# Performance work log

Hardware: AMD Instinct MI355X
Metric: run time of the kernel (lower is better)

Reference implementation:

```python
import jax, jax.numpy as jnp
import numpy as np

GRID_SIZE = 16          # number of spline intervals; G+1 = 17 control points
KH, KW = 3, 3           # kernel size
EPS = 1e-8


def _extract_patches(x, kh, kw):
    """x: (B,H,W,C) -> patches (B,Ho,Wo,C,kh,kw), valid padding, stride 1."""
    B, H, W, C = x.shape
    Ho, Wo = H - kh + 1, W - kw + 1
    rows = []
    for i in range(kh):
        cols = []
        for j in range(kw):
            cols.append(x[:, i:i + Ho, j:j + Wo, :])  # (B,Ho,Wo,C)
        rows.append(jnp.stack(cols, axis=-1))          # (B,Ho,Wo,C,kw)
    return jnp.stack(rows, axis=-2)                    # (B,Ho,Wo,C,kh,kw)


def setup_inputs() -> dict:
    key = jax.random.key(0)
    k1, k2, k3, k4 = jax.random.split(key, 4)
    B, H, W, C, F = 4, 66, 66, 32, 64
    x = jax.random.normal(k1, (B, H, W, C), dtype=jnp.float32)
    control_points = jax.random.normal(k2, (F, C, KH, KW, GRID_SIZE + 1), dtype=jnp.float32) * 0.1
    w_spline = jax.random.normal(k3, (F, C, KH, KW), dtype=jnp.float32) * 0.1
    w_silu = jax.random.normal(k4, (F, C, KH, KW), dtype=jnp.float32) * 0.1
    bias = jnp.zeros((F,), dtype=jnp.float32)
    return {"x": x, "control_points": control_points, "w_spline": w_spline,
            "w_silu": w_silu, "bias": bias}


def reference(x, control_points, w_spline, w_silu, bias):
    # Fixed B-spline grid in [-1, 1]
    grid = jnp.linspace(-1.0, 1.0, GRID_SIZE + 1, dtype=x.dtype)  # (G+1,)
    grid_spacing = 2.0 / GRID_SIZE

    # Patch extraction (valid padding, stride 1)
    patches = _extract_patches(x, KH, KW)  # (B,Ho,Wo,C,kh,kw)

    # Linear B-spline (hat) basis with normalization
    xc = jnp.clip(patches, -1.0, 1.0)
    dist = jnp.abs(xc[..., None] - grid)                     # (B,Ho,Wo,C,kh,kw,G+1)
    w = jnp.maximum(0.0, 1.0 - dist / grid_spacing)
    basis = w / (jnp.sum(w, axis=-1, keepdims=True) + EPS)

    # K(x) = w_spline * spline(x) + w_silu * SiLU(x); reduce over (C,kh,kw) per filter
    cp_eff = w_spline[..., None] * control_points            # (F,C,kh,kw,G+1)
    spline_term = jnp.einsum('bhwcijg,fcijg->bhwf', basis, cp_eff)
    silu_term = jnp.einsum('bhwcij,fcij->bhwf', jax.nn.silu(patches), w_silu)

    return spline_term + silu_term + bias  # (B,Ho,Wo,F)
```

## Files before the change

### kernel.cpp

```cpp
#include <hip/hip_runtime.h>
#include <stdint.h>

typedef _Float16 half8 __attribute__((ext_vector_type(8)));
typedef float f32x16 __attribute__((ext_vector_type(16)));

#define NPX  (4 * 66 * 66 * 32)
#define NTH  (3 * 64 * 1728)
#define TH_OFF_BYTES ((size_t)NPX * 18 * 2)
#define PREP_BLOCKS  ((NPX + NTH) / 256)

__global__ __launch_bounds__(256) void kan_prep(
    const float* __restrict__ x, const float* __restrict__ cp,
    const float* __restrict__ wspl, const float* __restrict__ wsil,
    _Float16* __restrict__ Ff, _Float16* __restrict__ th)
{
    int tid = blockIdx.x * 256 + threadIdx.x;
    if (tid < NPX) {
        float p  = x[tid];
        float xc = fminf(1.0f, fmaxf(-1.0f, p));
        float u  = fmaf(xc, 8.0f, 8.0f);
        union { _Float16 h[18]; uint32_t w[9]; } pk;
#pragma unroll
        for (int m = 0; m < 17; ++m)
            pk.h[m] = (_Float16)fmaxf(0.0f, 1.0f - fabsf(u - (float)m));
        pk.h[17] = (_Float16)(p * __builtin_amdgcn_rcpf(1.0f + __expf(-p)));
        uint32_t* dst = (uint32_t*)(Ff + (size_t)tid * 18);
#pragma unroll
        for (int q = 0; q < 9; ++q) dst[q] = pk.w[q];
    } else if (tid < NPX + NTH) {
        int e  = tid - NPX;
        int k  = e % 1728;
        int fi = e / 1728;
        int f  = fi & 63;
        int i  = fi >> 6;
        int j  = k / 576;
        int q  = k - j * 576;
        int c  = q / 18;
        int m  = q - c * 18;
        int base = ((f * 32 + c) * 3 + i) * 3 + j;
        float v = (m < 17) ? wspl[base] * cp[base * 17 + m] : wsil[base];
        th[e] = (_Float16)v;
    }
}

__global__ __launch_bounds__(128) void kan_main(
    const _Float16* __restrict__ Ff, const _Float16* __restrict__ th,
    const float* __restrict__ bias, float* __restrict__ out)
{
    __shared__ _Float16 lA[2][64 * 72];
    __shared__ _Float16 lB[2][64 * 72];

    const int bx = blockIdx.x;
    const int i  = blockIdx.y;
    const int b  = bx >> 6;
    const int ho = bx & 63;
    const int tid  = threadIdx.x;
    const int wv   = tid >> 6;
    const int lane = tid & 63;
    const int spx   = tid >> 1;
    const int shalf = tid & 1;

    const size_t Abase = (size_t)((b * 66 + ho + i) * 66) * 576;
    const size_t Bbase = (size_t)(i * 64 + spx) * 1728;

    uint4 pfA0, pfA1, pfA2, pfA3, pfB0, pfB1, pfB2, pfB3;
#define LOADCH(ch)                                                             \
    {                                                                          \
        int j_  = (ch) / 9;                                                    \
        int qo_ = ((ch) - j_ * 9) * 64;                                        \
        const uint4* ga = (const uint4*)(Ff + Abase + (size_t)(spx + j_) * 576 \
                                         + qo_ + shalf * 32);                  \
        pfA0 = ga[0]; pfA1 = ga[1]; pfA2 = ga[2]; pfA3 = ga[3];                \
        const uint4* gb = (const uint4*)(th + Bbase + (ch) * 64 + shalf * 32); \
        pfB0 = gb[0]; pfB1 = gb[1]; pfB2 = gb[2]; pfB3 = gb[3];                \
    }

    LOADCH(0)

    const int r31 = lane & 31, kh = lane >> 5;
    f32x16 acc0, acc1;
    {
        float b0v = (i == 1) ? bias[r31] : 0.0f;
        float b1v = (i == 1) ? bias[32 + r31] : 0.0f;
#pragma unroll
        for (int r = 0; r < 16; ++r) { acc0[r] = b0v; acc1[r] = b1v; }
    }

    const int aoff  = (wv * 32 + r31) * 72 + kh * 8;
    const int boff0 = r31 * 72 + kh * 8;
    const int boff1 = (32 + r31) * 72 + kh * 8;
    char* wbA = (char*)lA[0] + spx * 144 + shalf * 64;
    char* wbB = (char*)lB[0] + spx * 144 + shalf * 64;

    int cur = 0;
    for (int ch = 0; ch < 27; ++ch) {
        uint4* wA = (uint4*)(wbA + cur * 9216);
        uint4* wB = (uint4*)(wbB + cur * 9216);
        wA[0] = pfA0; wA[1] = pfA1; wA[2] = pfA2; wA[3] = pfA3;
        wB[0] = pfB0; wB[1] = pfB1; wB[2] = pfB2; wB[3] = pfB3;
        __syncthreads();
        if (ch < 26) LOADCH(ch + 1)
        const _Float16* pa  = lA[cur] + aoff;
        const _Float16* pb0 = lB[cur] + boff0;
        const _Float16* pb1 = lB[cur] + boff1;
#pragma unroll
        for (int s = 0; s < 4; ++s) {
            half8 a  = *(const half8*)(pa  + s * 16);
            half8 b0 = *(const half8*)(pb0 + s * 16);
            half8 b1 = *(const half8*)(pb1 + s * 16);
            acc0 = __builtin_amdgcn_mfma_f32_32x32x16_f16(a, b0, acc0, 0, 0, 0);
            acc1 = __builtin_amdgcn_mfma_f32_32x32x16_f16(a, b1, acc1, 0, 0, 0);
        }
        cur ^= 1;
    }
#undef LOADCH

    float* orow = out + ((size_t)(b * 64 + ho) * 64) * 64;
#pragma unroll
    for (int r = 0; r < 16; ++r) {
        int row = (r & 3) + 8 * (r >> 2) + 4 * kh;
        int wo  = wv * 32 + row;
        atomicAdd(orow + wo * 64 + r31,      acc0[r]);
        atomicAdd(orow + wo * 64 + 32 + r31, acc1[r]);
    }
}

extern "C" void kernel_launch(void* const* d_in, const int* in_sizes, int n_in,
                              void* d_out, int out_size, void* d_ws, size_t ws_size,
                              hipStream_t stream) {
    const float* x    = (const float*)d_in[0];
    const float* cp   = (const float*)d_in[1];
    const float* wspl = (const float*)d_in[2];
    const float* wsil = (const float*)d_in[3];
    const float* bias = (const float*)d_in[4];
    float* out = (float*)d_out;

    uint8_t* ws = (uint8_t*)d_ws;
    _Float16* Ff = (_Float16*)ws;
    _Float16* th = (_Float16*)(ws + TH_OFF_BYTES);

    kan_prep<<<PREP_BLOCKS, 256, 0, stream>>>(x, cp, wspl, wsil, Ff, th);
    hipMemsetAsync(d_out, 0, (size_t)out_size * 4, stream);

    dim3 grid(256, 3);
    kan_main<<<grid, 128, 0, stream>>>(Ff, th, bias, out);
}
```

Measured before the change: 107.3 us.

## Drop LDS staging; load MFMA operands directly from global with register prefetch

The main kernel no longer stages A and B tiles through double-buffered shared memory with barriers. Each wave now loads its MFMA operands straight from global memory into registers, prefetching the next chunk. The tile is halved so each wave computes one 32x32 output block, and the grid grows to 1536 one-dimensional blocks with the kernel-row index innermost. This removes LDS traffic and __syncthreads, at the cost of redundant global and L2 reads, since operands are no longer shared between the waves of a block.

```diff
diff --git a/kernel.cpp b/kernel.cpp
--- a/kernel.cpp
+++ b/kernel.cpp
@@ -47,81 +47,62 @@
     const _Float16* __restrict__ Ff, const _Float16* __restrict__ th,
     const float* __restrict__ bias, float* __restrict__ out)
 {
-    __shared__ _Float16 lA[2][64 * 72];
-    __shared__ _Float16 lB[2][64 * 72];
+    const int bid = blockIdx.x;
+    const int i  = bid % 3;
+    const int g  = bid / 3;
+    const int h2 = g & 1;
+    const int ho = (g >> 1) & 63;
+    const int b  = g >> 7;
 
-    const int bx = blockIdx.x;
-    const int i  = blockIdx.y;
-    const int b  = bx >> 6;
-    const int ho = bx & 63;
     const int tid  = threadIdx.x;
     const int wv   = tid >> 6;
     const int lane = tid & 63;
-    const int spx   = tid >> 1;
-    const int shalf = tid & 1;
+    const int r31  = lane & 31;
+    const int kh   = lane >> 5;
 
-    const size_t Abase = (size_t)((b * 66 + ho + i) * 66) * 576;
-    const size_t Bbase = (size_t)(i * 64 + spx) * 1728;
+    const _Float16* pA = Ff
+        + ((size_t)((b * 66 + ho + i) * 66 + h2 * 32 + r31)) * 576 + kh * 8;
+    const _Float16* pB = th
+        + ((size_t)(i * 64 + wv * 32 + r31)) * 1728 + kh * 8;
 
-    uint4 pfA0, pfA1, pfA2, pfA3, pfB0, pfB1, pfB2, pfB3;
-#define LOADCH(ch)                                                             \
-    {                                                                          \
-        int j_  = (ch) / 9;                                                    \
-        int qo_ = ((ch) - j_ * 9) * 64;                                        \
-        const uint4* ga = (const uint4*)(Ff + Abase + (size_t)(spx + j_) * 576 \
-                                         + qo_ + shalf * 32);                  \
-        pfA0 = ga[0]; pfA1 = ga[1]; pfA2 = ga[2]; pfA3 = ga[3];                \
-        const uint4* gb = (const uint4*)(th + Bbase + (ch) * 64 + shalf * 32); \
-        pfB0 = gb[0]; pfB1 = gb[1]; pfB2 = gb[2]; pfB3 = gb[3];                \
+    f32x16 acc;
+    {
+        float bv = (i == 1) ? bias[wv * 32 + r31] : 0.0f;
+#pragma unroll
+        for (int r = 0; r < 16; ++r) acc[r] = bv;
     }
 
-    LOADCH(0)
-
-    const int r31 = lane & 31, kh = lane >> 5;
-    f32x16 acc0, acc1;
-    {
-        float b0v = (i == 1) ? bias[r31] : 0.0f;
-        float b1v = (i == 1) ? bias[32 + r31] : 0.0f;
-#pragma unroll
-        for (int r = 0; r < 16; ++r) { acc0[r] = b0v; acc1[r] = b1v; }
+#define LD(t, A0, A1, A2, A3, B0, B1, B2, B3)                                  \
+    {                                                                          \
+        const _Float16* qa = pA + (t) * 64;                                    \
+        const _Float16* qb = pB + (t) * 64;                                    \
+        A0 = *(const half8*)(qa);      A1 = *(const half8*)(qa + 16);          \
+        A2 = *(const half8*)(qa + 32); A3 = *(const half8*)(qa + 48);          \
+        B0 = *(const half8*)(qb);      B1 = *(const half8*)(qb + 16);          \
+        B2 = *(const half8*)(qb + 32); B3 = *(const half8*)(qb + 48);          \
     }
 
-    const int aoff  = (wv * 32 + r31) * 72 + kh * 8;
-    const int boff0 = r31 * 72 + kh * 8;
-    const int boff1 = (32 + r31) * 72 + kh * 8;
-    char* wbA = (char*)lA[0] + spx * 144 + shalf * 64;
-    char* wbB = (char*)lB[0] + spx * 144 + shalf * 64;
+    half8 a0, a1, a2, a3, b0, b1, b2, b3;
+    half8 na0, na1, na2, na3, nb0, nb1, nb2, nb3;
+    LD(0, a0, a1, a2, a3, b0, b1, b2, b3)
 
-    int cur = 0;
-    for (int ch = 0; ch < 27; ++ch) {
-        uint4* wA = (uint4*)(wbA + cur * 9216);
-        uint4* wB = (uint4*)(wbB + cur * 9216);
-        wA[0] = pfA0; wA[1] = pfA1; wA[2] = pfA2; wA[3] = pfA3;
-        wB[0] = pfB0; wB[1] = pfB1; wB[2] = pfB2; wB[3] = pfB3;
-        __syncthreads();
-        if (ch < 26) LOADCH(ch + 1)
-        const _Float16* pa  = lA[cur] + aoff;
-        const _Float16* pb0 = lB[cur] + boff0;
-        const _Float16* pb1 = lB[cur] + boff1;
 #pragma unroll
-        for (int s = 0; s < 4; ++s) {
-            half8 a  = *(const half8*)(pa  + s * 16);
-            half8 b0 = *(const half8*)(pb0 + s * 16);
-            half8 b1 = *(const half8*)(pb1 + s * 16);
-            acc0 = __builtin_amdgcn_mfma_f32_32x32x16_f16(a, b0, acc0, 0, 0, 0);
-            acc1 = __builtin_amdgcn_mfma_f32_32x32x16_f16(a, b1, acc1, 0, 0, 0);
-        }
-        cur ^= 1;
+    for (int t = 0; t < 27; ++t) {
+        if (t < 26) LD(t + 1, na0, na1, na2, na3, nb0, nb1, nb2, nb3)
+        acc = __builtin_amdgcn_mfma_f32_32x32x16_f16(a0, b0, acc, 0, 0, 0);
+        acc = __builtin_amdgcn_mfma_f32_32x32x16_f16(a1, b1, acc, 0, 0, 0);
+        acc = __builtin_amdgcn_mfma_f32_32x32x16_f16(a2, b2, acc, 0, 0, 0);
+        acc = __builtin_amdgcn_mfma_f32_32x32x16_f16(a3, b3, acc, 0, 0, 0);
+        a0 = na0; a1 = na1; a2 = na2; a3 = na3;
+        b0 = nb0; b1 = nb1; b2 = nb2; b3 = nb3;
     }
-#undef LOADCH
+#undef LD
 
-    float* orow = out + ((size_t)(b * 64 + ho) * 64) * 64;
+    float* obase = out + ((size_t)((b * 64 + ho) * 64 + h2 * 32)) * 64 + wv * 32;
 #pragma unroll
     for (int r = 0; r < 16; ++r) {
-        int row = (r & 3) + 8 * (r >> 2) + 4 * kh;
-        int wo  = wv * 32 + row;
-        atomicAdd(orow + wo * 64 + r31,      acc0[r]);
-        atomicAdd(orow + wo * 64 + 32 + r31, acc1[r]);
+        int rowD = (r & 3) + 8 * (r >> 2) + 4 * kh;
+        atomicAdd(obase + (size_t)rowD * 64 + r31, acc[r]);
     }
 }
 
@@ -142,6 +123,5 @@
     kan_prep<<<PREP_BLOCKS, 256, 0, stream>>>(x, cp, wspl, wsil, Ff, th);
     hipMemsetAsync(d_out, 0, (size_t)out_size * 4, stream);
 
-    dim3 grid(256, 3);
-    kan_main<<<grid, 128, 0, stream>>>(Ff, th, bias, out);
+    kan_main<<<1536, 128, 0, stream>>>(Ff, th, bias, out);
 }
```

After: 161.9 us. 50.9% more time.
